# Kernel tuning notes

Hardware: AMD Instinct MI355X
Metric: run time of the kernel (lower is better)

## Reference

```python
import jax, jax.numpy as jnp
import numpy as np

N = 50000
E = 800000
G_DIM = 128
HEADS = 8
DEPTH = 3
EPS = 1e-5


def _ln(x, w, b):
    m = jnp.mean(x, axis=-1, keepdims=True)
    v = jnp.var(x, axis=-1, keepdims=True)
    return (x - m) * jax.lax.rsqrt(v + EPS) * w + b


def setup_inputs() -> dict:
    key = jax.random.key(0)
    ks = jax.random.split(key, 12)
    s = 0.02
    inp = {
        "h": jax.random.normal(ks[0], (N, G_DIM), jnp.float32),
        "src": jax.random.randint(ks[1], (E,), 0, N, jnp.int32),
        "dst": jax.random.randint(ks[2], (E,), 0, N, jnp.int32),
        # outer norm
        "norm_w": jnp.ones((G_DIM,), jnp.float32),
        "norm_b": jnp.zeros((G_DIM,), jnp.float32),
        # attention norm_in
        "nin_w": jnp.ones((G_DIM,), jnp.float32),
        "nin_b": jnp.zeros((G_DIM,), jnp.float32),
        # to_qkv (no bias)
        "Wqkv": jax.random.normal(ks[3], (G_DIM, 3 * G_DIM), jnp.float32) * s,
        # ff norm_out
        "no_w": jnp.ones((G_DIM,), jnp.float32),
        "no_b": jnp.zeros((G_DIM,), jnp.float32),
        # ff linears (hidden = 4*g_dim)
        "W1": jax.random.normal(ks[4], (G_DIM, 4 * G_DIM), jnp.float32) * s,
        "b1": jnp.zeros((4 * G_DIM,), jnp.float32),
        "W2": jax.random.normal(ks[5], (4 * G_DIM, G_DIM), jnp.float32) * s,
        "b2": jnp.zeros((G_DIM,), jnp.float32),
    }
    return inp


def _graph_attention(x, src, dst, nin_w, nin_b, Wqkv):
    # x: [N, g_dim]
    s = _ln(x, nin_w, nin_b)
    qkv = s @ Wqkv                                   # [N, 3*g_dim]
    q, k, v = jnp.split(qkv, 3, axis=-1)
    D = G_DIM // HEADS
    q = q.reshape(N, HEADS, D)
    k = k.reshape(N, HEADS, D)
    v = v.reshape(N, HEADS, D)
    scale = G_DIM ** (-0.5)
    # edge scores: elementwise q[src] * k[dst] per (head, dim) channel
    att = q[src] * k[dst] * scale                    # [E, H, D]
    # edge softmax over incoming edges of each dst node, per channel
    mx = jax.ops.segment_max(att, dst, num_segments=N)   # [N, H, D]
    e = jnp.exp(att - mx[dst])
    z = jax.ops.segment_sum(e, dst, num_segments=N)      # [N, H, D]
    a = e / z[dst]
    # weighted message aggregation
    rst = jax.ops.segment_sum(v[src] * a, dst, num_segments=N)  # [N, H, D]
    return rst.reshape(N, G_DIM)


def reference(h, src, dst, norm_w, norm_b, nin_w, nin_b, Wqkv,
              no_w, no_b, W1, b1, W2, b2):
    for _ in range(DEPTH):
        x = _ln(h, norm_w, norm_b)
        x = _graph_attention(x, src, dst, nin_w, nin_b, Wqkv)
        # feedforward with its own pre-norm
        y = _ln(x, no_w, no_b)
        y = jax.nn.gelu(y @ W1 + b1, approximate=False) @ W2 + b2
        h = y + h
    return h
```

## Files before the change

kernel.cpp:

```cpp
#include <hip/hip_runtime.h>
#include <math.h>

#define N_NODES 50000
#define N_EDGES 800000
#define EPS 1e-5f

#define SCAN_CHUNK 1024
#define SCAN_NBLK ((N_NODES + SCAN_CHUNK - 1) / SCAN_CHUNK)

typedef unsigned short u16;
typedef __attribute__((ext_vector_type(8))) u16 u16x8;
typedef __attribute__((ext_vector_type(8))) short bf16x8;
typedef __attribute__((ext_vector_type(4))) float f32x4;

__device__ __forceinline__ u16 f2bf(float x) {
  unsigned u = __float_as_uint(x);
  return (u16)((u + 0x7FFFu + ((u >> 16) & 1u)) >> 16);
}
__device__ __forceinline__ float bf2f(u16 b) {
  return __uint_as_float(((unsigned)b) << 16);
}

__global__ void count_kernel(const int* __restrict__ dst, int* __restrict__ cnt, int e_total) {
  int e = blockIdx.x * 256 + threadIdx.x;
  if (e < e_total) atomicAdd(&cnt[dst[e]], 1);
}

__global__ __launch_bounds__(256) void scan1_kernel(const int* __restrict__ cnt,
                                                    int* __restrict__ offs,
                                                    int* __restrict__ bsum, int n) {
  __shared__ int buf[256];
  int t = threadIdx.x;
  int base = blockIdx.x * SCAN_CHUNK + t * 4;
  int v0 = (base + 0 < n) ? cnt[base + 0] : 0;
  int v1 = (base + 1 < n) ? cnt[base + 1] : 0;
  int v2 = (base + 2 < n) ? cnt[base + 2] : 0;
  int v3 = (base + 3 < n) ? cnt[base + 3] : 0;
  int tsum = v0 + v1 + v2 + v3;
  buf[t] = tsum;
  __syncthreads();
  for (int st = 1; st < 256; st <<= 1) {
    int x = (t >= st) ? buf[t - st] : 0;
    __syncthreads();
    buf[t] += x;
    __syncthreads();
  }
  int texcl = buf[t] - tsum;
  if (base + 0 < n) offs[base + 0] = texcl;
  if (base + 1 < n) offs[base + 1] = texcl + v0;
  if (base + 2 < n) offs[base + 2] = texcl + v0 + v1;
  if (base + 3 < n) offs[base + 3] = texcl + v0 + v1 + v2;
  if (t == 255) bsum[blockIdx.x] = buf[255];
}

__global__ void scan2_kernel(const int* __restrict__ bsum, int* __restrict__ bbase) {
  int lane = threadIdx.x;
  int v = (lane < SCAN_NBLK) ? bsum[lane] : 0;
  int orig = v;
#pragma unroll
  for (int ofs = 1; ofs < 64; ofs <<= 1) {
    int u = __shfl_up(v, ofs, 64);
    if (lane >= ofs) v += u;
  }
  if (lane < SCAN_NBLK) bbase[lane] = v - orig;
}

__global__ __launch_bounds__(256) void scan3_kernel(int* __restrict__ offs,
                                                    int* __restrict__ cursor,
                                                    const int* __restrict__ bbase, int n) {
  int t = threadIdx.x;
  int b = bbase[blockIdx.x];
  int base = blockIdx.x * SCAN_CHUNK + t * 4;
#pragma unroll
  for (int j = 0; j < 4; ++j) {
    int i = base + j;
    if (i < n) {
      int o = offs[i] + b;
      offs[i] = o;
      cursor[i] = o;
    }
  }
  if (blockIdx.x == 0 && t == 0) offs[n] = N_EDGES;
}

__global__ void scatter_kernel(const int* __restrict__ src, const int* __restrict__ dst,
                               int* __restrict__ cursor, int* __restrict__ ssrc, int e_total) {
  int e = blockIdx.x * 256 + threadIdx.x;
  if (e < e_total) {
    int p = atomicAdd(&cursor[dst[e]], 1);
    ssrc[p] = src[e];
  }
}

__global__ void wsplit_kernel(const float* __restrict__ W, u16* __restrict__ outH,
                              u16* __restrict__ outL, int K, int M) {
  int e = blockIdx.x * 256 + threadIdx.x;
  if (e >= K * M) return;
  int n = e % M, k = e / M;
  float a = W[e];
  u16 hb = f2bf(a);
  outH[(size_t)n * K + k] = hb;
  outL[(size_t)n * K + k] = f2bf(a - bf2f(hb));
}

__device__ __forceinline__ float wave_sum(float v) {
#pragma unroll
  for (int m = 32; m > 0; m >>= 1) v += __shfl_xor(v, m, 64);
  return v;
}

__global__ __launch_bounds__(256) void ln2_kernel(
    const float* __restrict__ h,
    const float* __restrict__ w1, const float* __restrict__ b1,
    const float* __restrict__ w2, const float* __restrict__ b2,
    u16* __restrict__ s_hi, u16* __restrict__ s_lo, int n) {
  int lane = threadIdx.x & 63;
  int row = blockIdx.x * 4 + (threadIdx.x >> 6);
  if (row >= n) return;
  float2 v = ((const float2*)(h + (size_t)row * 128))[lane];
  float s = wave_sum(v.x + v.y);
  float q = wave_sum(v.x * v.x + v.y * v.y);
  float mean = s * (1.0f / 128.0f);
  float var = q * (1.0f / 128.0f) - mean * mean;
  float rs = 1.0f / sqrtf(var + EPS);
  float2 wv = ((const float2*)w1)[lane];
  float2 bv = ((const float2*)b1)[lane];
  float x0 = (v.x - mean) * rs * wv.x + bv.x;
  float x1 = (v.y - mean) * rs * wv.y + bv.y;
  float s2 = wave_sum(x0 + x1);
  float q2 = wave_sum(x0 * x0 + x1 * x1);
  float mean2 = s2 * (1.0f / 128.0f);
  float var2 = q2 * (1.0f / 128.0f) - mean2 * mean2;
  float rs2 = 1.0f / sqrtf(var2 + EPS);
  float2 wv2 = ((const float2*)w2)[lane];
  float2 bv2 = ((const float2*)b2)[lane];
  float o0 = (x0 - mean2) * rs2 * wv2.x + bv2.x;
  float o1 = (x1 - mean2) * rs2 * wv2.y + bv2.y;
  u16 h0 = f2bf(o0), h1 = f2bf(o1);
  u16 l0 = f2bf(o0 - bf2f(h0)), l1 = f2bf(o1 - bf2f(h1));
  ((unsigned*)s_hi)[(size_t)row * 64 + lane] = (unsigned)h0 | ((unsigned)h1 << 16);
  ((unsigned*)s_lo)[(size_t)row * 64 + lane] = (unsigned)l0 | ((unsigned)l1 << 16);
}

__global__ __launch_bounds__(256) void ln1_kernel(
    const float* __restrict__ h,
    const float* __restrict__ w1, const float* __restrict__ b1,
    u16* __restrict__ s_hi, u16* __restrict__ s_lo, int n) {
  int lane = threadIdx.x & 63;
  int row = blockIdx.x * 4 + (threadIdx.x >> 6);
  if (row >= n) return;
  float2 v = ((const float2*)(h + (size_t)row * 128))[lane];
  float s = wave_sum(v.x + v.y);
  float q = wave_sum(v.x * v.x + v.y * v.y);
  float mean = s * (1.0f / 128.0f);
  float var = q * (1.0f / 128.0f) - mean * mean;
  float rs = 1.0f / sqrtf(var + EPS);
  float2 wv = ((const float2*)w1)[lane];
  float2 bv = ((const float2*)b1)[lane];
  float o0 = (v.x - mean) * rs * wv.x + bv.x;
  float o1 = (v.y - mean) * rs * wv.y + bv.y;
  u16 h0 = f2bf(o0), h1 = f2bf(o1);
  u16 l0 = f2bf(o0 - bf2f(h0)), l1 = f2bf(o1 - bf2f(h1));
  ((unsigned*)s_hi)[(size_t)row * 64 + lane] = (unsigned)h0 | ((unsigned)h1 << 16);
  ((unsigned*)s_lo)[(size_t)row * 64 + lane] = (unsigned)l0 | ((unsigned)l1 << 16);
}

__global__ __launch_bounds__(256) void attn_kernel(
    const u16* __restrict__ qv, const float* __restrict__ kbuf,
    const int* __restrict__ offs, const int* __restrict__ ssrc,
    float* __restrict__ rst, int n) {
  int lane = threadIdx.x & 63;
  int node = blockIdx.x * 4 + (threadIdx.x >> 6);
  if (node >= n) return;
  const float SCALE = 0.08838834764831845f;
  float2 kc = ((const float2*)(kbuf + (size_t)node * 128))[lane];
  kc.x *= SCALE; kc.y *= SCALE;
  int e0 = offs[node], e1 = offs[node + 1];
  float z0 = 0.f, z1 = 0.f, a0 = 0.f, a1 = 0.f;
  int e = e0;
  for (; e + 1 < e1; e += 2) {
    int s0 = ssrc[e], s1 = ssrc[e + 1];
    ushort4 wa = ((const ushort4*)(qv + (size_t)s0 * 256))[lane];
    ushort4 wb = ((const ushort4*)(qv + (size_t)s1 * 256))[lane];
    float pa0 = __expf(bf2f(wa.x) * kc.x), pa1 = __expf(bf2f(wa.y) * kc.y);
    float pb0 = __expf(bf2f(wb.x) * kc.x), pb1 = __expf(bf2f(wb.y) * kc.y);
    z0 += pa0 + pb0;
    z1 += pa1 + pb1;
    a0 = fmaf(pa0, bf2f(wa.z), fmaf(pb0, bf2f(wb.z), a0));
    a1 = fmaf(pa1, bf2f(wa.w), fmaf(pb1, bf2f(wb.w), a1));
  }
  if (e < e1) {
    int s0 = ssrc[e];
    ushort4 wa = ((const ushort4*)(qv + (size_t)s0 * 256))[lane];
    float pa0 = __expf(bf2f(wa.x) * kc.x), pa1 = __expf(bf2f(wa.y) * kc.y);
    z0 += pa0; z1 += pa1;
    a0 = fmaf(pa0, bf2f(wa.z), a0);
    a1 = fmaf(pa1, bf2f(wa.w), a1);
  }
  float2 o;
  o.x = (e1 > e0) ? a0 / z0 : 0.f;
  o.y = (e1 > e0) ? a1 / z1 : 0.f;
  ((float2*)(rst + (size_t)node * 128))[lane] = o;
}

struct StageA { u16x8 a0h, a1h, a0l, a1l; };
struct StageB { u16x8 b0h, b0l, b1h, b1l; };

template <int ACT, bool SPLITA, int K>
__global__ __launch_bounds__(256) void gemm_split(
    const u16* __restrict__ Ah, const u16* __restrict__ Al,
    const u16* __restrict__ BhT, const u16* __restrict__ BlT,
    const float* __restrict__ bias, const float* __restrict__ res,
    float* __restrict__ outF, u16* __restrict__ outH,
    u16* __restrict__ qvb, float* __restrict__ kbuf,
    int nrows, int M) {
  __shared__ u16 Ae[2][128][72];
  __shared__ u16 Be[2][128][72];
  int tid = threadIdx.x;
  int lane = tid & 63;
  int wid = tid >> 6;
  int wr = wid >> 1, wc = wid & 1;
  int lr = lane & 15, lg = lane >> 4;
  int row0 = blockIdx.y * 128, col0 = blockIdx.x * 128;
  bool full_tile = (row0 + 128 <= nrows);

  f32x4 acc[4][4] = {};

  int ra0 = tid >> 2;
  int ka0 = (tid & 3) * 8;

  const int NT = K / 32;

  auto loadA = [&](int k0, StageA& r) {
    if (full_tile) {
      int gr = row0 + ra0;
      r.a0h = *(const u16x8*)(Ah + (size_t)gr * K + k0 + ka0);
      r.a1h = *(const u16x8*)(Ah + (size_t)(gr + 64) * K + k0 + ka0);
      if (SPLITA) {
        r.a0l = *(const u16x8*)(Al + (size_t)gr * K + k0 + ka0);
        r.a1l = *(const u16x8*)(Al + (size_t)(gr + 64) * K + k0 + ka0);
      }
    } else {
      int gr = row0 + ra0;
      r.a0h = (u16x8){}; r.a1h = (u16x8){}; r.a0l = (u16x8){}; r.a1l = (u16x8){};
      if (gr < nrows) {
        r.a0h = *(const u16x8*)(Ah + (size_t)gr * K + k0 + ka0);
        if (SPLITA) r.a0l = *(const u16x8*)(Al + (size_t)gr * K + k0 + ka0);
      }
      if (gr + 64 < nrows) {
        r.a1h = *(const u16x8*)(Ah + (size_t)(gr + 64) * K + k0 + ka0);
        if (SPLITA) r.a1l = *(const u16x8*)(Al + (size_t)(gr + 64) * K + k0 + ka0);
      }
    }
  };
  auto loadB = [&](int k0, StageB& r) {
    int gc = col0 + ra0;
    r.b0h = *(const u16x8*)(BhT + (size_t)gc * K + k0 + ka0);
    r.b0l = *(const u16x8*)(BlT + (size_t)gc * K + k0 + ka0);
    r.b1h = *(const u16x8*)(BhT + (size_t)(gc + 64) * K + k0 + ka0);
    r.b1l = *(const u16x8*)(BlT + (size_t)(gc + 64) * K + k0 + ka0);
  };
  auto writeLDS = [&](int buf, const StageA& a, const StageB& b) {
    *(u16x8*)&Ae[buf][ra0][ka0] = a.a0h;
    *(u16x8*)&Ae[buf][ra0 + 64][ka0] = a.a1h;
    if (SPLITA) {
      *(u16x8*)&Ae[buf][ra0][32 + ka0] = a.a0l;
      *(u16x8*)&Ae[buf][ra0 + 64][32 + ka0] = a.a1l;
    }
    *(u16x8*)&Be[buf][ra0][ka0] = b.b0h;
    *(u16x8*)&Be[buf][ra0][32 + ka0] = b.b0l;
    *(u16x8*)&Be[buf][ra0 + 64][ka0] = b.b1h;
    *(u16x8*)&Be[buf][ra0 + 64][32 + ka0] = b.b1l;
  };

  StageA ar; StageB br;
  loadA(0, ar); loadB(0, br);
  writeLDS(0, ar, br);
  __syncthreads();

#pragma unroll
  for (int t = 0; t < NT; ++t) {
    int cur = t & 1;
    if (t + 1 < NT) {
      loadA((t + 1) * 32, ar);
      loadB((t + 1) * 32, br);
    }
    bf16x8 afh[4], afl[4], bfh[4], bfl[4];
#pragma unroll
    for (int mi = 0; mi < 4; ++mi) {
      afh[mi] = *(const bf16x8*)&Ae[cur][wr * 64 + mi * 16 + lr][lg * 8];
      if (SPLITA) afl[mi] = *(const bf16x8*)&Ae[cur][wr * 64 + mi * 16 + lr][32 + lg * 8];
    }
#pragma unroll
    for (int ni = 0; ni < 4; ++ni) {
      bfh[ni] = *(const bf16x8*)&Be[cur][wc * 64 + ni * 16 + lr][lg * 8];
      bfl[ni] = *(const bf16x8*)&Be[cur][wc * 64 + ni * 16 + lr][32 + lg * 8];
    }
#pragma unroll
    for (int mi = 0; mi < 4; ++mi)
#pragma unroll
      for (int ni = 0; ni < 4; ++ni) {
        acc[mi][ni] = __builtin_amdgcn_mfma_f32_16x16x32_bf16(afh[mi], bfh[ni], acc[mi][ni], 0, 0, 0);
        if (SPLITA)
          acc[mi][ni] = __builtin_amdgcn_mfma_f32_16x16x32_bf16(afl[mi], bfh[ni], acc[mi][ni], 0, 0, 0);
        acc[mi][ni] = __builtin_amdgcn_mfma_f32_16x16x32_bf16(afh[mi], bfl[ni], acc[mi][ni], 0, 0, 0);
      }
    if (t + 1 < NT) writeLDS(cur ^ 1, ar, br);
    __syncthreads();
  }

#pragma unroll
  for (int mi = 0; mi < 4; ++mi) {
#pragma unroll
    for (int j = 0; j < 4; ++j) {
      int r = row0 + wr * 64 + mi * 16 + lg * 4 + j;
      if (!full_tile && r >= nrows) continue;
#pragma unroll
      for (int ni = 0; ni < 4; ++ni) {
        int c = col0 + wc * 64 + ni * 16 + lr;
        float v = acc[mi][ni][j];
        if (ACT == 0) {
          if (c < 128) {
            qvb[(size_t)r * 256 + ((c >> 1) << 2) + (c & 1)] = f2bf(v);
          } else if (c < 256) {
            kbuf[(size_t)r * 128 + (c - 128)] = v;
          } else {
            int cc = c - 256;
            qvb[(size_t)r * 256 + ((cc >> 1) << 2) + 2 + (cc & 1)] = f2bf(v);
          }
        } else if (ACT == 1) {
          v += bias[c];
          v = 0.5f * v * (1.0f + erff(v * 0.70710678118654752f));
          outH[(size_t)r * M + c] = f2bf(v);
        } else {
          v += bias[c] + res[(size_t)r * M + c];
          outF[(size_t)r * M + c] = v;
        }
      }
    }
  }
}

extern "C" void kernel_launch(void* const* d_in, const int* in_sizes, int n_in,
                              void* d_out, int out_size, void* d_ws, size_t ws_size,
                              hipStream_t stream) {
  const float* h_in   = (const float*)d_in[0];
  const int*   src    = (const int*)d_in[1];
  const int*   dst    = (const int*)d_in[2];
  const float* norm_w = (const float*)d_in[3];
  const float* norm_b = (const float*)d_in[4];
  const float* nin_w  = (const float*)d_in[5];
  const float* nin_b  = (const float*)d_in[6];
  const float* Wqkv   = (const float*)d_in[7];
  const float* no_w   = (const float*)d_in[8];
  const float* no_b   = (const float*)d_in[9];
  const float* W1     = (const float*)d_in[10];
  const float* b1     = (const float*)d_in[11];
  const float* W2     = (const float*)d_in[12];
  const float* b2     = (const float*)d_in[13];
  float* out = (float*)d_out;

  char* wsp = (char*)d_ws;
  float* h_cur = (float*)wsp;             wsp += (size_t)N_NODES * 128 * 4;
  u16* s_hi = (u16*)wsp;                  wsp += (size_t)N_NODES * 128 * 2;
  u16* s_lo = (u16*)wsp;                  wsp += (size_t)N_NODES * 128 * 2;
  u16* qvb  = (u16*)wsp;                  wsp += (size_t)N_NODES * 256 * 2;
  float* kbuf = (float*)wsp;              wsp += (size_t)N_NODES * 128 * 4;
  u16* hid  = (u16*)wsp;                  wsp += (size_t)N_NODES * 512 * 2;
  u16* WqT_h = (u16*)wsp; wsp += 49152 * 2;
  u16* WqT_l = (u16*)wsp; wsp += 49152 * 2;
  u16* W1T_h = (u16*)wsp; wsp += 65536 * 2;
  u16* W1T_l = (u16*)wsp; wsp += 65536 * 2;
  u16* W2T_h = (u16*)wsp; wsp += 65536 * 2;
  u16* W2T_l = (u16*)wsp; wsp += 65536 * 2;
  int* cnt    = (int*)wsp;
  int* cursor = cnt + N_NODES;
  int* offs   = cursor + N_NODES;
  int* ssrc   = offs + N_NODES + 1;
  int* bsum   = ssrc + N_EDGES;
  int* bbase  = bsum + 64;

  hipMemsetAsync(cnt, 0, N_NODES * sizeof(int), stream);
  count_kernel<<<(N_EDGES + 255) / 256, 256, 0, stream>>>(dst, cnt, N_EDGES);
  scan1_kernel<<<SCAN_NBLK, 256, 0, stream>>>(cnt, offs, bsum, N_NODES);
  scan2_kernel<<<1, 64, 0, stream>>>(bsum, bbase);
  scan3_kernel<<<SCAN_NBLK, 256, 0, stream>>>(offs, cursor, bbase, N_NODES);
  scatter_kernel<<<(N_EDGES + 255) / 256, 256, 0, stream>>>(src, dst, cursor, ssrc, N_EDGES);

  wsplit_kernel<<<(128 * 384 + 255) / 256, 256, 0, stream>>>(Wqkv, WqT_h, WqT_l, 128, 384);
  wsplit_kernel<<<(128 * 512 + 255) / 256, 256, 0, stream>>>(W1, W1T_h, W1T_l, 128, 512);
  wsplit_kernel<<<(512 * 128 + 255) / 256, 256, 0, stream>>>(W2, W2T_h, W2T_l, 512, 128);

  const int grid_rows = (N_NODES + 127) / 128;

  for (int layer = 0; layer < 3; ++layer) {
    const float* h_src = (layer == 0) ? h_in : h_cur;
    float* h_dst = (layer == 2) ? out : h_cur;

    ln2_kernel<<<12500, 256, 0, stream>>>(h_src, norm_w, norm_b, nin_w, nin_b, s_hi, s_lo, N_NODES);
    gemm_split<0, true, 128><<<dim3(3, grid_rows), 256, 0, stream>>>(
        s_hi, s_lo, WqT_h, WqT_l, nullptr, nullptr,
        nullptr, nullptr, qvb, kbuf, N_NODES, 384);
    attn_kernel<<<12500, 256, 0, stream>>>(qvb, kbuf, offs, ssrc, out, N_NODES);
    ln1_kernel<<<12500, 256, 0, stream>>>(out, no_w, no_b, s_hi, s_lo, N_NODES);
    gemm_split<1, true, 128><<<dim3(4, grid_rows), 256, 0, stream>>>(
        s_hi, s_lo, W1T_h, W1T_l, b1, nullptr,
        nullptr, hid, nullptr, nullptr, N_NODES, 512);
    gemm_split<2, false, 512><<<dim3(1, grid_rows), 256, 0, stream>>>(
        hid, nullptr, W2T_h, W2T_l, b2, h_src,
        h_dst, nullptr, nullptr, nullptr, N_NODES, 128);
  }
}
```

Before: 861.7 us.

## Stage GEMM tiles with direct global-to-LDS async loads in fragment-ready layout

Replaces the register-staged global-to-LDS copy in the split-bf16 GEMM with global_load_lds async loads that write each 16x32 sub-tile straight into LDS, laid out so each lane's MFMA fragment is contiguous. LDS moves to dynamic shared memory sized per variant, and the K loop is unrolled by 2 instead of fully. This is meant to cut register pressure and the VGPR round trip during prefetch, and to simplify LDS reads. In exchange it relies on the async load ordering being covered by the existing barrier (no explicit vmcnt wait is visible), clamps out-of-range rows to the last row instead of zero-filling, and removes padding, so LDS bank conflicts may change.

```diff
diff --git a/kernel.cpp b/kernel.cpp
--- a/kernel.cpp
+++ b/kernel.cpp
@@ -19,6 +19,12 @@
 }
 __device__ __forceinline__ float bf2f(u16 b) {
   return __uint_as_float(((unsigned)b) << 16);
+}
+
+__device__ __forceinline__ void async_ld16(u16* lds, const u16* g) {
+  __builtin_amdgcn_global_load_lds(
+      (const __attribute__((address_space(1))) unsigned int*)g,
+      (__attribute__((address_space(3))) unsigned int*)lds, 16, 0, 0);
 }
 
 __global__ void count_kernel(const int* __restrict__ dst, int* __restrict__ cnt, int e_total) {
@@ -203,9 +209,6 @@
   ((float2*)(rst + (size_t)node * 128))[lane] = o;
 }
 
-struct StageA { u16x8 a0h, a1h, a0l, a1l; };
-struct StageB { u16x8 b0h, b0l, b1h, b1l; };
-
 template <int ACT, bool SPLITA, int K>
 __global__ __launch_bounds__(256) void gemm_split(
     const u16* __restrict__ Ah, const u16* __restrict__ Al,
@@ -214,8 +217,10 @@
     float* __restrict__ outF, u16* __restrict__ outH,
     u16* __restrict__ qvb, float* __restrict__ kbuf,
     int nrows, int M) {
-  __shared__ u16 Ae[2][128][72];
-  __shared__ u16 Be[2][128][72];
+  extern __shared__ u16 smem[];
+  constexpr int PLANE = 4096;
+  constexpr int SBUF = (SPLITA ? 4 : 3) * PLANE;
+  constexpr int NT = K / 32;
   int tid = threadIdx.x;
   int lane = tid & 63;
   int wid = tid >> 6;
@@ -223,78 +228,43 @@
   int lr = lane & 15, lg = lane >> 4;
   int row0 = blockIdx.y * 128, col0 = blockIdx.x * 128;
   bool full_tile = (row0 + 128 <= nrows);
+  int kb8 = lg * 8;
 
   f32x4 acc[4][4] = {};
 
-  int ra0 = tid >> 2;
-  int ka0 = (tid & 3) * 8;
-
-  const int NT = K / 32;
-
-  auto loadA = [&](int k0, StageA& r) {
-    if (full_tile) {
-      int gr = row0 + ra0;
-      r.a0h = *(const u16x8*)(Ah + (size_t)gr * K + k0 + ka0);
-      r.a1h = *(const u16x8*)(Ah + (size_t)(gr + 64) * K + k0 + ka0);
-      if (SPLITA) {
-        r.a0l = *(const u16x8*)(Al + (size_t)gr * K + k0 + ka0);
-        r.a1l = *(const u16x8*)(Al + (size_t)(gr + 64) * K + k0 + ka0);
-      }
-    } else {
-      int gr = row0 + ra0;
-      r.a0h = (u16x8){}; r.a1h = (u16x8){}; r.a0l = (u16x8){}; r.a1l = (u16x8){};
-      if (gr < nrows) {
-        r.a0h = *(const u16x8*)(Ah + (size_t)gr * K + k0 + ka0);
-        if (SPLITA) r.a0l = *(const u16x8*)(Al + (size_t)gr * K + k0 + ka0);
-      }
-      if (gr + 64 < nrows) {
-        r.a1h = *(const u16x8*)(Ah + (size_t)(gr + 64) * K + k0 + ka0);
-        if (SPLITA) r.a1l = *(const u16x8*)(Al + (size_t)(gr + 64) * K + k0 + ka0);
-      }
+  auto stage = [&](int buf, int k0) {
+    u16* base = smem + buf * SBUF;
+#pragma unroll
+    for (int i = 0; i < 2; ++i) {
+      int sub = wid * 2 + i;
+      int arow = min(row0 + sub * 16 + lr, nrows - 1);
+      int bcol = col0 + sub * 16 + lr;
+      async_ld16(base + sub * 512, Ah + (size_t)arow * K + k0 + kb8);
+      async_ld16(base + PLANE + sub * 512, BhT + (size_t)bcol * K + k0 + kb8);
+      async_ld16(base + 2 * PLANE + sub * 512, BlT + (size_t)bcol * K + k0 + kb8);
+      if (SPLITA)
+        async_ld16(base + 3 * PLANE + sub * 512, Al + (size_t)arow * K + k0 + kb8);
     }
   };
-  auto loadB = [&](int k0, StageB& r) {
-    int gc = col0 + ra0;
-    r.b0h = *(const u16x8*)(BhT + (size_t)gc * K + k0 + ka0);
-    r.b0l = *(const u16x8*)(BlT + (size_t)gc * K + k0 + ka0);
-    r.b1h = *(const u16x8*)(BhT + (size_t)(gc + 64) * K + k0 + ka0);
-    r.b1l = *(const u16x8*)(BlT + (size_t)(gc + 64) * K + k0 + ka0);
-  };
-  auto writeLDS = [&](int buf, const StageA& a, const StageB& b) {
-    *(u16x8*)&Ae[buf][ra0][ka0] = a.a0h;
-    *(u16x8*)&Ae[buf][ra0 + 64][ka0] = a.a1h;
-    if (SPLITA) {
-      *(u16x8*)&Ae[buf][ra0][32 + ka0] = a.a0l;
-      *(u16x8*)&Ae[buf][ra0 + 64][32 + ka0] = a.a1l;
-    }
-    *(u16x8*)&Be[buf][ra0][ka0] = b.b0h;
-    *(u16x8*)&Be[buf][ra0][32 + ka0] = b.b0l;
-    *(u16x8*)&Be[buf][ra0 + 64][ka0] = b.b1h;
-    *(u16x8*)&Be[buf][ra0 + 64][32 + ka0] = b.b1l;
-  };
-
-  StageA ar; StageB br;
-  loadA(0, ar); loadB(0, br);
-  writeLDS(0, ar, br);
+
+  stage(0, 0);
   __syncthreads();
 
-#pragma unroll
+#pragma unroll 2
   for (int t = 0; t < NT; ++t) {
     int cur = t & 1;
-    if (t + 1 < NT) {
-      loadA((t + 1) * 32, ar);
-      loadB((t + 1) * 32, br);
-    }
+    if (t + 1 < NT) stage(cur ^ 1, (t + 1) * 32);
+    const u16* base = smem + cur * SBUF;
     bf16x8 afh[4], afl[4], bfh[4], bfl[4];
 #pragma unroll
     for (int mi = 0; mi < 4; ++mi) {
-      afh[mi] = *(const bf16x8*)&Ae[cur][wr * 64 + mi * 16 + lr][lg * 8];
-      if (SPLITA) afl[mi] = *(const bf16x8*)&Ae[cur][wr * 64 + mi * 16 + lr][32 + lg * 8];
+      afh[mi] = *(const bf16x8*)(base + (wr * 4 + mi) * 512 + lane * 8);
+      if (SPLITA) afl[mi] = *(const bf16x8*)(base + 3 * PLANE + (wr * 4 + mi) * 512 + lane * 8);
     }
 #pragma unroll
     for (int ni = 0; ni < 4; ++ni) {
-      bfh[ni] = *(const bf16x8*)&Be[cur][wc * 64 + ni * 16 + lr][lg * 8];
-      bfl[ni] = *(const bf16x8*)&Be[cur][wc * 64 + ni * 16 + lr][32 + lg * 8];
+      bfh[ni] = *(const bf16x8*)(base + PLANE + (wc * 4 + ni) * 512 + lane * 8);
+      bfl[ni] = *(const bf16x8*)(base + 2 * PLANE + (wc * 4 + ni) * 512 + lane * 8);
     }
 #pragma unroll
     for (int mi = 0; mi < 4; ++mi)
@@ -305,7 +275,6 @@
           acc[mi][ni] = __builtin_amdgcn_mfma_f32_16x16x32_bf16(afl[mi], bfh[ni], acc[mi][ni], 0, 0, 0);
         acc[mi][ni] = __builtin_amdgcn_mfma_f32_16x16x32_bf16(afh[mi], bfl[ni], acc[mi][ni], 0, 0, 0);
       }
-    if (t + 1 < NT) writeLDS(cur ^ 1, ar, br);
     __syncthreads();
   }
 
@@ -392,21 +361,23 @@
   wsplit_kernel<<<(512 * 128 + 255) / 256, 256, 0, stream>>>(W2, W2T_h, W2T_l, 512, 128);
 
   const int grid_rows = (N_NODES + 127) / 128;
+  constexpr size_t SH_SPLIT = 2u * 4 * 4096 * 2;
+  constexpr size_t SH_NOSPLIT = 2u * 3 * 4096 * 2;
 
   for (int layer = 0; layer < 3; ++layer) {
     const float* h_src = (layer == 0) ? h_in : h_cur;
     float* h_dst = (layer == 2) ? out : h_cur;
 
     ln2_kernel<<<12500, 256, 0, stream>>>(h_src, norm_w, norm_b, nin_w, nin_b, s_hi, s_lo, N_NODES);
-    gemm_split<0, true, 128><<<dim3(3, grid_rows), 256, 0, stream>>>(
+    gemm_split<0, true, 128><<<dim3(3, grid_rows), 256, SH_SPLIT, stream>>>(
         s_hi, s_lo, WqT_h, WqT_l, nullptr, nullptr,
         nullptr, nullptr, qvb, kbuf, N_NODES, 384);
     attn_kernel<<<12500, 256, 0, stream>>>(qvb, kbuf, offs, ssrc, out, N_NODES);
     ln1_kernel<<<12500, 256, 0, stream>>>(out, no_w, no_b, s_hi, s_lo, N_NODES);
-    gemm_split<1, true, 128><<<dim3(4, grid_rows), 256, 0, stream>>>(
+    gemm_split<1, true, 128><<<dim3(4, grid_rows), 256, SH_SPLIT, stream>>>(
         s_hi, s_lo, W1T_h, W1T_l, b1, nullptr,
         nullptr, hid, nullptr, nullptr, N_NODES, 512);
-    gemm_split<2, false, 512><<<dim3(1, grid_rows), 256, 0, stream>>>(
+    gemm_split<2, false, 512><<<dim3(1, grid_rows), 256, SH_NOSPLIT, stream>>>(
         hid, nullptr, W2T_h, W2T_l, b2, h_src,
         h_dst, nullptr, nullptr, nullptr, N_NODES, 128);
   }
```

After: 918.0 us. 1.07x slower.
